# Performance work log

Hardware: AMD Instinct MI355X
Metric: run time of the kernel (lower is better)

The kernel has to match this reference:

```python
import jax, jax.numpy as jnp
import numpy as np
from jax import lax

HEADS = 8
C, H, W = 64, 16, 16
D_K = C // HEADS
SCALE = 1.0 / np.sqrt(D_K * H * W).astype(np.float32)


def conv2d(x, w, b):
    # x: [N, C, H, W], w: [O, I, 3, 3], padding=1
    y = lax.conv_general_dilated(x, w, window_strides=(1, 1),
                                 padding=((1, 1), (1, 1)),
                                 dimension_numbers=('NCHW', 'OIHW', 'NCHW'))
    return y + b[None, :, None, None]


def _project(x, w, b, bs, seq):
    # x: [bs, seq, C, H, W] -> conv per frame -> [bs, heads, seq, d_k*H*W]
    y = conv2d(x.reshape(bs * seq, C, H, W), w, b)
    y = y.reshape(bs, seq, HEADS, D_K, H, W)
    y = jnp.transpose(y, (0, 2, 1, 3, 4, 5)).reshape(bs, HEADS, seq, D_K * H * W)
    return y


def setup_inputs() -> dict:
    key = jax.random.key(0)
    ks = jax.random.split(key, 11)
    shp = (2, 256, C, H, W)
    wstd = 1.0 / np.sqrt(C * 9)  # torch Conv2d default init scale
    inp = {
        'q': jax.random.normal(ks[0], shp, jnp.float32),
        'k': jax.random.normal(ks[1], shp, jnp.float32),
        'v': jax.random.normal(ks[2], shp, jnp.float32),
        'Wq': jax.random.uniform(ks[3], (C, C, 3, 3), jnp.float32, -wstd, wstd),
        'bq': jax.random.uniform(ks[4], (C,), jnp.float32, -wstd, wstd),
        'Wk': jax.random.uniform(ks[5], (C, C, 3, 3), jnp.float32, -wstd, wstd),
        'bk': jax.random.uniform(ks[6], (C,), jnp.float32, -wstd, wstd),
        'Wv': jax.random.uniform(ks[7], (C, C, 3, 3), jnp.float32, -wstd, wstd),
        'bv': jax.random.uniform(ks[8], (C,), jnp.float32, -wstd, wstd),
        'Wo': jax.random.uniform(ks[9], (C, C, 3, 3), jnp.float32, -wstd, wstd),
        'bo': jax.random.uniform(ks[10], (C,), jnp.float32, -wstd, wstd),
    }
    return inp


def reference(q, k, v, Wq, bq, Wk, bk, Wv, bv, Wo, bo):
    bs, seq = q.shape[0], q.shape[1]
    qh = _project(q, Wq, bq, bs, seq)  # [bs, h, seq, d_k*H*W]
    kh = _project(k, Wk, bk, bs, seq)
    vh = _project(v, Wv, bv, bs, seq)
    scores = jnp.einsum('bhqd,bhkd->bhqk', qh, kh) * SCALE
    attn = jax.nn.softmax(scores, axis=-1)
    out = jnp.einsum('bhqk,bhkd->bhqd', attn, vh)  # [bs, h, seq, d_k*H*W]
    out = out.reshape(bs, HEADS, seq, D_K, H, W)
    concat = jnp.transpose(out, (0, 2, 1, 3, 4, 5)).reshape(bs * seq, C, H, W)
    y = conv2d(concat, Wo, bo).reshape(bs, seq, C, H, W)
    return y
```

## Files before the change

kernel.cpp:

```cpp
#include <hip/hip_runtime.h>
#include <hip/hip_bf16.h>
#include <hip/hip_fp16.h>

typedef unsigned short u16;
typedef _Float16 f16x8 __attribute__((ext_vector_type(8)));
typedef u16 u16x8 __attribute__((ext_vector_type(8)));
typedef u16 u16x4 __attribute__((ext_vector_type(4)));
typedef float f32x4 __attribute__((ext_vector_type(4)));

__device__ __forceinline__ u16 f2h(float f){
  __half h = __float2half(f);
  return *(u16*)&h;
}

__device__ __forceinline__ void cp16_async(const u16* g, u16* l){
  __builtin_amdgcn_global_load_lds(
      (const __attribute__((address_space(1))) unsigned int*)g,
      (__attribute__((address_space(3))) unsigned int*)l,
      16, 0, 0);
}

__device__ __forceinline__ void prep_w_body(const float* W, u16* Wt, int i){
  if (i >= 36864) return;
  int co = i / 576, rem = i % 576, ci = rem / 9, tap = rem % 9;
  int n = co >> 4, lr = co & 15, kk = ci >> 5, lg = (ci >> 3) & 3, j = ci & 7;
  int s = tap*2 + kk;
  Wt[(((s*4 + n)*64) + lg*16 + lr)*8 + j] = f2h(W[i]);
}

__global__ __launch_bounds__(256) void prep_w3(
    const float* __restrict__ Wq, const float* __restrict__ Wk,
    const float* __restrict__ Wv, u16* __restrict__ Wt)
{
  int which = blockIdx.y;
  const float* W = (which == 0) ? Wq : (which == 1) ? Wk : Wv;
  prep_w_body(W, Wt + which*36864, blockIdx.x * 256 + threadIdx.x);
}

__global__ __launch_bounds__(256) void prep_w(
    const float* __restrict__ W, u16* __restrict__ Wt)
{
  prep_w_body(W, Wt, blockIdx.x * 256 + threadIdx.x);
}

template<bool IN_F32, bool OUT_PROJ>
__device__ __forceinline__ void conv_body(
    const void* __restrict__ xin, const u16* __restrict__ Wt,
    const float* __restrict__ bias, void* __restrict__ dst,
    int frame, u16* xT, float* stage, int tid)
{
  #define STAGE_H(h) do {                                                   \
    if (IN_F32){                                                            \
      const float* src_ = (const float*)xin + (size_t)frame*16384 + (h)*8192; \
      _Pragma("unroll")                                                     \
      for (int t_ = 0; t_ < 4; ++t_){                                       \
        int c_ = tid + t_*512;                                              \
        cp16_async((const u16*)(src_ + c_*4), (u16*)(stage + c_*4));        \
      }                                                                     \
    } else {                                                                \
      const u16* src_ = (const u16*)xin + (size_t)frame*16384 + (h)*8192;   \
      _Pragma("unroll")                                                     \
      for (int t_ = 0; t_ < 2; ++t_){                                       \
        int c_ = tid + t_*512;                                              \
        cp16_async(src_ + c_*8, (u16*)stage + c_*8);                        \
      }                                                                     \
    }                                                                       \
  } while(0)

  const int p = tid & 255, ph = tid >> 8;
  const int py = p >> 4, px = p & 15;
  const int pp = (py + 1)*18 + px + 1;

  #define TRANSP(h) do {                                                    \
    const float* Sf_ = stage;                                               \
    const u16*   Su_ = (const u16*)stage;                                   \
    _Pragma("unroll")                                                       \
    for (int t_ = 0; t_ < 2; ++t_){                                         \
      int cbl_ = ph*2 + t_;                                                 \
      u16x8 pk_;                                                            \
      _Pragma("unroll")                                                     \
      for (int j_ = 0; j_ < 8; ++j_){                                       \
        int cl_ = cbl_*8 + j_;                                              \
        pk_[j_] = IN_F32 ? f2h(Sf_[cl_*256 + p]) : Su_[cl_*256 + p];        \
      }                                                                     \
      unsigned cb_ = (unsigned)((h)*4 + cbl_);                              \
      unsigned off_ = (unsigned)(pp*128) + (((cb_ + (unsigned)pp) & 7u) << 4); \
      *(u16x8*)((char*)xT + off_) = pk_;                                    \
    }                                                                       \
  } while(0)

  const int w = tid >> 6, lane = tid & 63, lr = lane & 15, lg = lane >> 4;
  const int pyb = w * 2;

  f32x4 acc[2][4];
  #pragma unroll
  for (int n = 0; n < 4; ++n){
    float b = bias[n*16 + lr];
    #pragma unroll
    for (int m = 0; m < 2; ++m){
      acc[m][n][0] = b; acc[m][n][1] = b; acc[m][n][2] = b; acc[m][n][3] = b;
    }
  }

  #define LOADB(s, B) do {                                                  \
    _Pragma("unroll")                                                       \
    for (int n_ = 0; n_ < 4; ++n_)                                          \
      B[n_] = *(const f16x8*)(Wt + ((((s)*4 + n_)*64) + lane)*8);           \
  } while(0)

  #define STEP(s, B) do {                                                   \
    int tap_ = (s) >> 1, kk_ = (s) & 1;                                     \
    int dy_ = tap_ / 3, dx_ = tap_ - dy_*3;                                 \
    f16x8 af_[2];                                                           \
    _Pragma("unroll")                                                       \
    for (int m_ = 0; m_ < 2; ++m_){                                         \
      int pp_ = (pyb + m_ + dy_)*18 + lr + dx_;                             \
      unsigned slot_ = ((unsigned)(kk_*4 + lg) + (unsigned)pp_) & 7u;       \
      af_[m_] = *(const f16x8*)((const char*)xT                             \
                 + (unsigned)(pp_*128) + (slot_ << 4));                     \
    }                                                                       \
    _Pragma("unroll")                                                       \
    for (int m_ = 0; m_ < 2; ++m_)                                          \
      _Pragma("unroll")                                                     \
      for (int n_ = 0; n_ < 4; ++n_)                                        \
        acc[m_][n_] = __builtin_amdgcn_mfma_f32_16x16x32_f16(               \
            af_[m_], B[n_], acc[m_][n_], 0, 0, 0);                          \
  } while(0)

  #define KLOOP(kk) do {                                                    \
    f16x8 Ba[4], Bb[4];                                                     \
    LOADB((kk), Ba);                                                        \
    _Pragma("unroll")                                                       \
    for (int tap = 0; tap < 9; ++tap){                                      \
      if (tap & 1){                                                         \
        if (tap + 1 < 9) LOADB(((tap+1)*2 + (kk)), Ba);                     \
        STEP((tap*2 + (kk)), Bb);                                           \
      } else {                                                              \
        if (tap + 1 < 9) LOADB(((tap+1)*2 + (kk)), Bb);                     \
        STEP((tap*2 + (kk)), Ba);                                           \
      }                                                                     \
    }                                                                       \
  } while(0)

  STAGE_H(0);
  for (int i = tid; i < 2592; i += 512)
    *(uint4*)((char*)xT + i*16) = make_uint4(0u, 0u, 0u, 0u);
  __syncthreads();

  TRANSP(0);
  __syncthreads();

  STAGE_H(1);
  KLOOP(0);
  __syncthreads();

  TRANSP(1);
  __syncthreads();

  KLOOP(1);

  #undef STAGE_H
  #undef TRANSP
  #undef LOADB
  #undef STEP
  #undef KLOOP

  if (OUT_PROJ){
    u16* d = (u16*)dst;
    const int b = frame >> 8, sq = frame & 255;
    #pragma unroll
    for (int n = 0; n < 4; ++n){
      int co = n*16 + lr, h = co >> 3, dk = co & 7;
      size_t base = ((size_t)((b*8 + h)*256 + sq))*2048 + dk*256;
      #pragma unroll
      for (int m = 0; m < 2; ++m){
        int P = w*32 + m*16 + lg*4;
        u16x4 o4;
        #pragma unroll
        for (int r = 0; r < 4; ++r) o4[r] = f2h(acc[m][n][r]);
        *(u16x4*)(d + base + P) = o4;
      }
    }
  } else {
    float* d = (float*)dst + (size_t)frame * 16384;
    #pragma unroll
    for (int n = 0; n < 4; ++n){
      int co = n*16 + lr;
      #pragma unroll
      for (int m = 0; m < 2; ++m){
        int P = w*32 + m*16 + lg*4;
        *(f32x4*)(d + co*256 + P) = acc[m][n];
      }
    }
  }
}

__global__ __launch_bounds__(512, 4) void conv3_mfma(
    const float* __restrict__ q, const float* __restrict__ k,
    const float* __restrict__ v, const u16* __restrict__ Wt3,
    const float* __restrict__ bq, const float* __restrict__ bk,
    const float* __restrict__ bv,
    u16* __restrict__ qh, u16* __restrict__ kh, u16* __restrict__ vh)
{
  __shared__ __align__(16) u16 xT[324 * 64];
  __shared__ __align__(16) float stage[8192];
  const int which = blockIdx.x >> 9;
  const int frame = blockIdx.x & 511;
  const float* x = (which == 0) ? q : (which == 1) ? k : v;
  const float* bias = (which == 0) ? bq : (which == 1) ? bk : bv;
  u16* dst = (which == 0) ? qh : (which == 1) ? kh : vh;
  conv_body<true, true>(x, Wt3 + which*36864, bias, dst, frame, xT, stage, threadIdx.x);
}

__global__ __launch_bounds__(512, 4) void conv_out_mfma(
    const u16* __restrict__ xin, const u16* __restrict__ Wt,
    const float* __restrict__ bias, float* __restrict__ out)
{
  __shared__ __align__(16) u16 xT[324 * 64];
  __shared__ __align__(16) float stage[8192];
  conv_body<false, false>(xin, Wt, bias, out, blockIdx.x, xT, stage, threadIdx.x);
}

__global__ __launch_bounds__(256) void transpose_v(
    const u16* __restrict__ vh, u16* __restrict__ vt)
{
  __shared__ u16 tile[64][72];
  const int tid = threadIdx.x;
  const int dt = blockIdx.x, st = blockIdx.y, bh = blockIdx.z;
  {
    int r = tid >> 2, c4 = tid & 3;
    const u16* src = vh + ((size_t)(bh*256 + st*64 + r))*2048 + dt*64 + c4*16;
    uint4 v0 = *(const uint4*)src;
    uint4 v1 = *(const uint4*)(src + 8);
    *(uint4*)&tile[r][c4*16]     = v0;
    *(uint4*)&tile[r][c4*16 + 8] = v1;
  }
  __syncthreads();
  {
    int dr = tid >> 2, s4 = tid & 3;
    u16 tmp[16];
    #pragma unroll
    for (int i = 0; i < 16; ++i) tmp[i] = tile[s4*16 + i][dr];
    u16* dstp = vt + ((size_t)(bh*2048 + dt*64 + dr))*256 + st*64 + s4*16;
    *(uint4*)dstp       = *(uint4*)&tmp[0];
    *(uint4*)(dstp + 8) = *(uint4*)&tmp[8];
  }
}

__global__ __launch_bounds__(512, 2) void attn_kernel(
    const u16* __restrict__ qh, const u16* __restrict__ kh,
    const u16* __restrict__ vt, u16* __restrict__ obuf)
{
  const float SCALE = 0.022097086912079608f;
  __shared__ __align__(16) u16 Qs[16*2048];
  __shared__ __align__(16) u16 Kb[2][16384];
  __shared__ __align__(16) u16 P[16*256];
  __shared__ float redA[8][16];
  __shared__ float redB[8][16];

  const int tid = threadIdx.x;
  const int w = tid >> 6, lane = tid & 63, lr = lane & 15, lg = lane >> 4;

  const int id = blockIdx.x;
  const int xcd = id & 7, j = id >> 3;
  const int bh = xcd + 8*(j & 1), qt = j >> 1;
  const int q0 = qt * 16, b = bh >> 3, h = bh & 7;

  const u16* Qg = qh + ((size_t)(bh*256 + q0))*2048;
  const u16* Kg = kh + (size_t)bh * 256 * 2048;
  const u16* Vg = vt + (size_t)bh * 2048 * 256;

  const int spK = (lane & 7) ^ ((lane >> 3) & 7);
  #define STAGE_K(c, buf)                                                   \
    _Pragma("unroll")                                                       \
    for (int r_ = 0; r_ < 4; ++r_)                                          \
      cp16_async(Kg + (size_t)(w*32 + r_*8 + (lane>>3))*2048 + (c)*64 + spK*8, \
                 (buf) + w*2048 + r_*512);

  #define STAGE_V(c, buf)                                                   \
    _Pragma("unroll")                                                       \
    for (int r_ = 0; r_ < 8; ++r_){                                         \
      int rl_ = w*16 + r_*2 + (lane>>5);                                    \
      int sp_ = (lane & 31) ^ (rl_ & 7);                                    \
      cp16_async(Vg + (size_t)((c)*128 + rl_)*256 + sp_*8,                  \
                 (buf) + w*4096 + r_*512);                                  \
    }

  #pragma unroll
  for (int r = 0; r < 8; ++r){
    int t = r*64 + lane;
    int row = w*2 + (t >> 8);
    int dp = t & 255;
    int sp = (dp & ~7) | ((dp & 7) ^ (row & 7));
    cp16_async(Qg + (size_t)row*2048 + sp*8, Qs + w*4096 + r*512);
  }
  STAGE_K(0, Kb[0]);
  __syncthreads();

  const f32x4 zero4 = {0.f, 0.f, 0.f, 0.f};
  f32x4 sacc[2] = {zero4, zero4};
  #pragma unroll 1
  for (int c = 0; c < 32; ++c){
    if (c < 31) STAGE_K(c+1, Kb[(c+1)&1]);
    const u16* kb = Kb[c&1];
    #pragma unroll
    for (int d2 = 0; d2 < 2; ++d2){
      unsigned aoff = (((unsigned)lr << 12) + (unsigned)(c*128 + d2*64 + lg*16))
                      ^ (unsigned)((lr & 7) << 4);
      f16x8 a = *(const f16x8*)((const char*)Qs + aoff);
      #pragma unroll
      for (int n = 0; n < 2; ++n){
        int row = w*32 + n*16 + lr;
        const u16* kp = kb + row*64 + (((d2*4 + lg) ^ (row & 7)) << 3);
        f16x8 bk = *(const f16x8*)kp;
        sacc[n] = __builtin_amdgcn_mfma_f32_16x16x32_f16(a, bk, sacc[n], 0,0,0);
      }
    }
    __syncthreads();
  }

  float mx[4];
  #pragma unroll
  for (int r = 0; r < 4; ++r){
    float vv = fmaxf(sacc[0][r], sacc[1][r]);
    #pragma unroll
    for (int off = 1; off < 16; off <<= 1) vv = fmaxf(vv, __shfl_xor(vv, off));
    mx[r] = vv;
  }
  if (lr == 0){
    #pragma unroll
    for (int r = 0; r < 4; ++r) redA[w][lg*4 + r] = mx[r];
  }
  __syncthreads();
  #pragma unroll
  for (int r = 0; r < 4; ++r){
    int row = lg*4 + r;
    float vv = redA[0][row];
    #pragma unroll
    for (int ww = 1; ww < 8; ++ww) vv = fmaxf(vv, redA[ww][row]);
    mx[r] = vv;
  }

  const int kbase = w * 32;
  float sm[4] = {0.f, 0.f, 0.f, 0.f};
  #pragma unroll
  for (int n = 0; n < 2; ++n)
    #pragma unroll
    for (int r = 0; r < 4; ++r){
      float pv = __expf((sacc[n][r] - mx[r]) * SCALE);
      sm[r] += pv;
      int row = lg*4 + r;
      int col = kbase + n*16 + lr;
      unsigned off = (((unsigned)row << 9) + ((unsigned)col << 1))
                     ^ (unsigned)((row & 7) << 4);
      *(u16*)((char*)P + off) = f2h(pv);
    }
  #pragma unroll
  for (int r = 0; r < 4; ++r){
    float vv = sm[r];
    #pragma unroll
    for (int off = 1; off < 16; off <<= 1) vv += __shfl_xor(vv, off);
    sm[r] = vv;
  }
  if (lr == 0){
    #pragma unroll
    for (int r = 0; r < 4; ++r) redB[w][lg*4 + r] = sm[r];
  }
  __syncthreads();
  float rs[4];
  #pragma unroll
  for (int r = 0; r < 4; ++r){
    int row = lg*4 + r;
    float s = redB[0][row];
    #pragma unroll
    for (int ww = 1; ww < 8; ++ww) s += redB[ww][row];
    rs[r] = 1.0f / s;
  }

  u16* Vb0 = Qs;
  u16* Vb1 = &Kb[0][0];
  STAGE_V(0, Vb0);
  __syncthreads();
  #pragma unroll 1
  for (int c = 0; c < 16; ++c){
    if (c < 15){
      u16* nbuf = ((c+1) & 1) ? Vb1 : Vb0;
      STAGE_V(c+1, nbuf);
    }
    const u16* vb = (c & 1) ? Vb1 : Vb0;
    f32x4 oacc = zero4;
    #pragma unroll
    for (int kt = 0; kt < 8; ++kt){
      unsigned poff = (((unsigned)lr << 9) + (unsigned)(kt*64 + lg*16))
                      ^ (unsigned)((lr & 7) << 4);
      f16x8 pa = *(const f16x8*)((const char*)P + poff);
      int row = w*16 + lr;
      const u16* vp = vb + row*256 + (((kt*4 + lg) ^ (row & 7)) << 3);
      f16x8 bv = *(const f16x8*)vp;
      oacc = __builtin_amdgcn_mfma_f32_16x16x32_f16(pa, bv, oacc, 0,0,0);
    }
    #pragma unroll
    for (int r = 0; r < 4; ++r){
      float o = oacc[r] * rs[r];
      int qrow = q0 + lg*4 + r;
      int d = c*128 + w*16 + lr;
      int frame = b*256 + qrow;
      int cdim = h*8 + (d >> 8);
      obuf[((size_t)(frame*64 + cdim))*256 + (d & 255)] = f2h(o);
    }
    __syncthreads();
  }
  #undef STAGE_K
  #undef STAGE_V
}

extern "C" void kernel_launch(void* const* d_in, const int* in_sizes, int n_in,
                              void* d_out, int out_size, void* d_ws, size_t ws_size,
                              hipStream_t stream)
{
  const float* q  = (const float*)d_in[0];
  const float* k  = (const float*)d_in[1];
  const float* v  = (const float*)d_in[2];
  const float* Wq = (const float*)d_in[3];
  const float* bq = (const float*)d_in[4];
  const float* Wk = (const float*)d_in[5];
  const float* bk = (const float*)d_in[6];
  const float* Wv = (const float*)d_in[7];
  const float* bv = (const float*)d_in[8];
  const float* Wo = (const float*)d_in[9];
  const float* bo = (const float*)d_in[10];
  float* out = (float*)d_out;

  char* ws = (char*)d_ws;
  u16* qh = (u16*)(ws);
  u16* kh = (u16*)(ws + (size_t)16*1024*1024);
  u16* vh = (u16*)(ws + (size_t)32*1024*1024);
  u16* vt = (u16*)(ws + (size_t)48*1024*1024);
  u16* obuf = vh;
  u16* Wt3  = vt;
  u16* WtO  = qh;

  prep_w3<<<dim3(144, 3), dim3(256), 0, stream>>>(Wq, Wk, Wv, Wt3);
  conv3_mfma<<<dim3(1536), dim3(512), 0, stream>>>(q, k, v, Wt3, bq, bk, bv,
                                                   qh, kh, vh);
  transpose_v<<<dim3(32, 4, 16), dim3(256), 0, stream>>>(vh, vt);
  attn_kernel<<<dim3(256), dim3(512), 0, stream>>>(qh, kh, vt, obuf);
  prep_w<<<dim3(144), dim3(256), 0, stream>>>(Wo, WtO);
  conv_out_mfma<<<dim3(512), dim3(512), 0, stream>>>(obuf, WtO, bo, out);
}
```

Baseline: 130.5 us.

## Process three frames per conv block with cross-frame double-buffered staging

The input-projection conv kernel now loops over three consecutive frames per block, launching a third as many blocks. Staging is split into quarter-channel chunks across two buffers, so the next frame's loads are issued while the current frame's second K-half computes. The weight-load pipeline is also deepened from two to three register buffers. The aim is to hide global-load latency and amortize xT zeroing and block launch, at the cost of fewer blocks to fill the GPU and more register pressure.

New measurement: 140.3 us. +7.5%, slower.

```diff
diff --git a/kernel.cpp b/kernel.cpp
--- a/kernel.cpp
+++ b/kernel.cpp
@@ -43,79 +43,63 @@
   prep_w_body(W, Wt, blockIdx.x * 256 + threadIdx.x);
 }
 
-template<bool IN_F32, bool OUT_PROJ>
-__device__ __forceinline__ void conv_body(
-    const void* __restrict__ xin, const u16* __restrict__ Wt,
-    const float* __restrict__ bias, void* __restrict__ dst,
-    int frame, u16* xT, float* stage, int tid)
-{
-  #define STAGE_H(h) do {                                                   \
+template<bool IN_F32, bool OUT_PROJ, int F>
+__device__ __forceinline__ void conv_frames(
+    const void* x0, const void* x1, const void* x2,
+    const u16* Wt_base, int wt_stride,
+    const float* b0, const float* b1, const float* b2,
+    void* d0, void* d1, void* d2,
+    int gf0, u16* xT, char* S0, char* S1, int tid)
+{
+  const int p = tid & 255, ph = tid >> 8;
+  const int py = p >> 4, px = p & 15;
+  const int pp = (py + 1)*18 + px + 1;
+  const int w = tid >> 6, lane = tid & 63, lr = lane & 15, lg = lane >> 4;
+  const int pyb = w * 2;
+
+  #define STAGE_Q(g, q, buf) do {                                           \
+    int w_ = (g) >> 9, fr_ = (g) & 511;                                     \
+    const void* xs_ = (w_ == 0) ? x0 : (w_ == 1) ? x1 : x2;                 \
     if (IN_F32){                                                            \
-      const float* src_ = (const float*)xin + (size_t)frame*16384 + (h)*8192; \
-      _Pragma("unroll")                                                     \
-      for (int t_ = 0; t_ < 4; ++t_){                                       \
-        int c_ = tid + t_*512;                                              \
-        cp16_async((const u16*)(src_ + c_*4), (u16*)(stage + c_*4));        \
-      }                                                                     \
-    } else {                                                                \
-      const u16* src_ = (const u16*)xin + (size_t)frame*16384 + (h)*8192;   \
+      const float* src_ = (const float*)xs_ + (size_t)fr_*16384 + (q)*4096; \
       _Pragma("unroll")                                                     \
       for (int t_ = 0; t_ < 2; ++t_){                                       \
         int c_ = tid + t_*512;                                              \
-        cp16_async(src_ + c_*8, (u16*)stage + c_*8);                        \
+        cp16_async((const u16*)(src_ + c_*4), (u16*)((buf) + c_*16));       \
       }                                                                     \
+    } else {                                                                \
+      const u16* src_ = (const u16*)xs_ + (size_t)fr_*16384 + (q)*4096;     \
+      cp16_async(src_ + tid*8, (u16*)((buf) + tid*16));                     \
     }                                                                       \
   } while(0)
 
-  const int p = tid & 255, ph = tid >> 8;
-  const int py = p >> 4, px = p & 15;
-  const int pp = (py + 1)*18 + px + 1;
-
-  #define TRANSP(h) do {                                                    \
-    const float* Sf_ = stage;                                               \
-    const u16*   Su_ = (const u16*)stage;                                   \
-    _Pragma("unroll")                                                       \
-    for (int t_ = 0; t_ < 2; ++t_){                                         \
-      int cbl_ = ph*2 + t_;                                                 \
-      u16x8 pk_;                                                            \
-      _Pragma("unroll")                                                     \
-      for (int j_ = 0; j_ < 8; ++j_){                                       \
-        int cl_ = cbl_*8 + j_;                                              \
-        pk_[j_] = IN_F32 ? f2h(Sf_[cl_*256 + p]) : Su_[cl_*256 + p];        \
-      }                                                                     \
-      unsigned cb_ = (unsigned)((h)*4 + cbl_);                              \
-      unsigned off_ = (unsigned)(pp*128) + (((cb_ + (unsigned)pp) & 7u) << 4); \
-      *(u16x8*)((char*)xT + off_) = pk_;                                    \
+  #define TRANSP(q, buf) do {                                               \
+    const float* Sf_ = (const float*)(buf);                                 \
+    const u16*   Su_ = (const u16*)(buf);                                   \
+    u16x8 pk_;                                                              \
+    _Pragma("unroll")                                                       \
+    for (int j_ = 0; j_ < 8; ++j_){                                         \
+      int cl_ = ph*8 + j_;                                                  \
+      pk_[j_] = IN_F32 ? f2h(Sf_[cl_*256 + p]) : Su_[cl_*256 + p];          \
     }                                                                       \
+    unsigned cb_ = (unsigned)((q)*2 + ph);                                  \
+    unsigned off_ = (unsigned)(pp*128) + (((cb_ + (unsigned)pp) & 7u) << 4);\
+    *(u16x8*)((char*)xT + off_) = pk_;                                      \
   } while(0)
 
-  const int w = tid >> 6, lane = tid & 63, lr = lane & 15, lg = lane >> 4;
-  const int pyb = w * 2;
-
-  f32x4 acc[2][4];
-  #pragma unroll
-  for (int n = 0; n < 4; ++n){
-    float b = bias[n*16 + lr];
-    #pragma unroll
-    for (int m = 0; m < 2; ++m){
-      acc[m][n][0] = b; acc[m][n][1] = b; acc[m][n][2] = b; acc[m][n][3] = b;
-    }
-  }
-
-  #define LOADB(s, B) do {                                                  \
+  #define LOADB(tap, kk, B) do {                                            \
     _Pragma("unroll")                                                       \
     for (int n_ = 0; n_ < 4; ++n_)                                          \
-      B[n_] = *(const f16x8*)(Wt + ((((s)*4 + n_)*64) + lane)*8);           \
+      B[n_] = *(const f16x8*)(Wt + (((((tap)*2+(kk))*4 + n_)*64) + lane)*8);\
   } while(0)
 
-  #define STEP(s, B) do {                                                   \
-    int tap_ = (s) >> 1, kk_ = (s) & 1;                                     \
-    int dy_ = tap_ / 3, dx_ = tap_ - dy_*3;                                 \
+  #define STEP(tap, kk, B) do {                                             \
+    int dy_ = (tap) / 3, dx_ = (tap) - dy_*3;                               \
     f16x8 af_[2];                                                           \
     _Pragma("unroll")                                                       \
     for (int m_ = 0; m_ < 2; ++m_){                                         \
       int pp_ = (pyb + m_ + dy_)*18 + lr + dx_;                             \
-      unsigned slot_ = ((unsigned)(kk_*4 + lg) + (unsigned)pp_) & 7u;       \
+      unsigned slot_ = ((unsigned)((kk)*4 + lg) + (unsigned)pp_) & 7u;      \
       af_[m_] = *(const f16x8*)((const char*)xT                             \
                  + (unsigned)(pp_*128) + (slot_ << 4));                     \
     }                                                                       \
@@ -128,71 +112,96 @@
   } while(0)
 
   #define KLOOP(kk) do {                                                    \
-    f16x8 Ba[4], Bb[4];                                                     \
-    LOADB((kk), Ba);                                                        \
-    _Pragma("unroll")                                                       \
-    for (int tap = 0; tap < 9; ++tap){                                      \
-      if (tap & 1){                                                         \
-        if (tap + 1 < 9) LOADB(((tap+1)*2 + (kk)), Ba);                     \
-        STEP((tap*2 + (kk)), Bb);                                           \
-      } else {                                                              \
-        if (tap + 1 < 9) LOADB(((tap+1)*2 + (kk)), Bb);                     \
-        STEP((tap*2 + (kk)), Ba);                                           \
-      }                                                                     \
-    }                                                                       \
+    f16x8 Ba[4], Bb[4], Bc[4];                                              \
+    LOADB(0,(kk),Ba); LOADB(1,(kk),Bb);                                     \
+    LOADB(2,(kk),Bc); STEP(0,(kk),Ba);                                      \
+    LOADB(3,(kk),Ba); STEP(1,(kk),Bb);                                      \
+    LOADB(4,(kk),Bb); STEP(2,(kk),Bc);                                      \
+    LOADB(5,(kk),Bc); STEP(3,(kk),Ba);                                      \
+    LOADB(6,(kk),Ba); STEP(4,(kk),Bb);                                      \
+    LOADB(7,(kk),Bb); STEP(5,(kk),Bc);                                      \
+    LOADB(8,(kk),Bc); STEP(6,(kk),Ba);                                      \
+    STEP(7,(kk),Bb);                                                        \
+    STEP(8,(kk),Bc);                                                        \
   } while(0)
 
-  STAGE_H(0);
+  STAGE_Q(gf0, 0, S0);
+  STAGE_Q(gf0, 1, S1);
   for (int i = tid; i < 2592; i += 512)
     *(uint4*)((char*)xT + i*16) = make_uint4(0u, 0u, 0u, 0u);
   __syncthreads();
 
-  TRANSP(0);
-  __syncthreads();
-
-  STAGE_H(1);
-  KLOOP(0);
-  __syncthreads();
-
-  TRANSP(1);
-  __syncthreads();
-
-  KLOOP(1);
-
-  #undef STAGE_H
+  #pragma unroll 1
+  for (int fi = 0; fi < F; ++fi){
+    const int gf = gf0 + fi;
+    const int which = gf >> 9, frame = gf & 511;
+    const u16* Wt = Wt_base + which*wt_stride;
+    const float* bias = (which == 0) ? b0 : (which == 1) ? b1 : b2;
+
+    TRANSP(0, S0);
+    TRANSP(1, S1);
+    __syncthreads();
+
+    STAGE_Q(gf, 2, S0);
+    STAGE_Q(gf, 3, S1);
+
+    f32x4 acc[2][4];
+    #pragma unroll
+    for (int n = 0; n < 4; ++n){
+      float b = bias[n*16 + lr];
+      #pragma unroll
+      for (int m = 0; m < 2; ++m){
+        acc[m][n][0] = b; acc[m][n][1] = b; acc[m][n][2] = b; acc[m][n][3] = b;
+      }
+    }
+    KLOOP(0);
+    __syncthreads();
+
+    TRANSP(2, S0);
+    TRANSP(3, S1);
+    __syncthreads();
+
+    if (fi + 1 < F){
+      STAGE_Q(gf + 1, 0, S0);
+      STAGE_Q(gf + 1, 1, S1);
+    }
+    KLOOP(1);
+
+    if (OUT_PROJ){
+      u16* d = (u16*)((which == 0) ? d0 : (which == 1) ? d1 : d2);
+      const int b = frame >> 8, sq = frame & 255;
+      #pragma unroll
+      for (int n = 0; n < 4; ++n){
+        int co = n*16 + lr, h = co >> 3, dk = co & 7;
+        size_t base = ((size_t)((b*8 + h)*256 + sq))*2048 + dk*256;
+        #pragma unroll
+        for (int m = 0; m < 2; ++m){
+          int P = w*32 + m*16 + lg*4;
+          u16x4 o4;
+          #pragma unroll
+          for (int r = 0; r < 4; ++r) o4[r] = f2h(acc[m][n][r]);
+          *(u16x4*)(d + base + P) = o4;
+        }
+      }
+    } else {
+      float* d = (float*)d0 + (size_t)frame * 16384;
+      #pragma unroll
+      for (int n = 0; n < 4; ++n){
+        int co = n*16 + lr;
+        #pragma unroll
+        for (int m = 0; m < 2; ++m){
+          int P = w*32 + m*16 + lg*4;
+          *(f32x4*)(d + co*256 + P) = acc[m][n];
+        }
+      }
+    }
+    if (fi + 1 < F) __syncthreads();
+  }
+  #undef STAGE_Q
   #undef TRANSP
   #undef LOADB
   #undef STEP
   #undef KLOOP
-
-  if (OUT_PROJ){
-    u16* d = (u16*)dst;
-    const int b = frame >> 8, sq = frame & 255;
-    #pragma unroll
-    for (int n = 0; n < 4; ++n){
-      int co = n*16 + lr, h = co >> 3, dk = co & 7;
-      size_t base = ((size_t)((b*8 + h)*256 + sq))*2048 + dk*256;
-      #pragma unroll
-      for (int m = 0; m < 2; ++m){
-        int P = w*32 + m*16 + lg*4;
-        u16x4 o4;
-        #pragma unroll
-        for (int r = 0; r < 4; ++r) o4[r] = f2h(acc[m][n][r]);
-        *(u16x4*)(d + base + P) = o4;
-      }
-    }
-  } else {
-    float* d = (float*)dst + (size_t)frame * 16384;
-    #pragma unroll
-    for (int n = 0; n < 4; ++n){
-      int co = n*16 + lr;
-      #pragma unroll
-      for (int m = 0; m < 2; ++m){
-        int P = w*32 + m*16 + lg*4;
-        *(f32x4*)(d + co*256 + P) = acc[m][n];
-      }
-    }
-  }
 }
 
 __global__ __launch_bounds__(512, 4) void conv3_mfma(
@@ -203,13 +212,10 @@
     u16* __restrict__ qh, u16* __restrict__ kh, u16* __restrict__ vh)
 {
   __shared__ __align__(16) u16 xT[324 * 64];
-  __shared__ __align__(16) float stage[8192];
-  const int which = blockIdx.x >> 9;
-  const int frame = blockIdx.x & 511;
-  const float* x = (which == 0) ? q : (which == 1) ? k : v;
-  const float* bias = (which == 0) ? bq : (which == 1) ? bk : bv;
-  u16* dst = (which == 0) ? qh : (which == 1) ? kh : vh;
-  conv_body<true, true>(x, Wt3 + which*36864, bias, dst, frame, xT, stage, threadIdx.x);
+  __shared__ __align__(16) char S0[16384];
+  __shared__ __align__(16) char S1[16384];
+  conv_frames<true, true, 3>(q, k, v, Wt3, 36864, bq, bk, bv,
+                             qh, kh, vh, blockIdx.x * 3, xT, S0, S1, threadIdx.x);
 }
 
 __global__ __launch_bounds__(512, 4) void conv_out_mfma(
@@ -217,8 +223,10 @@
     const float* __restrict__ bias, float* __restrict__ out)
 {
   __shared__ __align__(16) u16 xT[324 * 64];
-  __shared__ __align__(16) float stage[8192];
-  conv_body<false, false>(xin, Wt, bias, out, blockIdx.x, xT, stage, threadIdx.x);
+  __shared__ __align__(16) char S0[16384];
+  __shared__ __align__(16) char S1[16384];
+  conv_frames<false, false, 1>(xin, xin, xin, Wt, 0, bias, bias, bias,
+                               out, out, out, blockIdx.x, xT, S0, S1, threadIdx.x);
 }
 
 __global__ __launch_bounds__(256) void transpose_v(
@@ -441,8 +449,8 @@
   u16* WtO  = qh;
 
   prep_w3<<<dim3(144, 3), dim3(256), 0, stream>>>(Wq, Wk, Wv, Wt3);
-  conv3_mfma<<<dim3(1536), dim3(512), 0, stream>>>(q, k, v, Wt3, bq, bk, bv,
-                                                   qh, kh, vh);
+  conv3_mfma<<<dim3(512), dim3(512), 0, stream>>>(q, k, v, Wt3, bq, bk, bv,
+                                                  qh, kh, vh);
   transpose_v<<<dim3(32, 4, 16), dim3(256), 0, stream>>>(vh, vt);
   attn_kernel<<<dim3(256), dim3(512), 0, stream>>>(qh, kh, vt, obuf);
   prep_w<<<dim3(144), dim3(256), 0, stream>>>(Wo, WtO);
```
